# Performance work log

Hardware: AMD Instinct MI355X
Metric: run time of the kernel (lower is better)

The kernel has to match this reference:

```python
import jax, jax.numpy as jnp
import numpy as np

B, S, H, L = 1, 2048, 2048, 2
NH, D_NOPE, D_ROPE, D_V = 16, 128, 64, 128
Q_RANK, KV_RANK = 1024, 512
E, K_TOP, I_FF, N_SHARED = 8, 2, 1408, 2
VOCAB, P_DIM = 32000, 4096
EPS = 1e-6
ROPE_BASE = 10000.0
D_QK = D_NOPE + D_ROPE  # 192


def rmsnorm(x, w):
    xf = x.astype(jnp.float32)
    var = jnp.mean(xf * xf, axis=-1, keepdims=True)
    return (w * (xf * jax.lax.rsqrt(var + EPS))).astype(x.dtype)


def rotate_half(x):
    d = x.shape[-1] // 2
    return jnp.concatenate([-x[..., d:], x[..., :d]], axis=-1)


def rope_tables(seq_len):
    inv_freq = 1.0 / (ROPE_BASE ** (jnp.arange(0, D_ROPE, 2, dtype=jnp.float32) / D_ROPE))
    t = jnp.arange(seq_len, dtype=jnp.float32)
    freqs = jnp.outer(t, inv_freq)                      # [S, D_ROPE/2]
    emb = jnp.concatenate([freqs, freqs], axis=-1)      # [S, D_ROPE]
    return jnp.cos(emb)[None, None], jnp.sin(emb)[None, None]  # [1,1,S,D_ROPE]


def mla_attention(x, qd, qn, qu, kvd, kvn, kvu, ow, cos, sin):
    b, s, _ = x.shape
    # low-rank Q path
    q = rmsnorm(x @ qd, qn) @ qu                        # [B,S,NH*D_QK]
    q = q.reshape(b, s, NH, D_QK).transpose(0, 2, 1, 3)  # [B,NH,S,D_QK]
    q_nope, q_rope = q[..., :D_NOPE], q[..., D_NOPE:]
    # low-rank KV path
    kv = x @ kvd                                        # [B,S,KV_RANK+D_ROPE]
    kv_latent, k_rope = kv[..., :KV_RANK], kv[..., KV_RANK:]
    kv_up = rmsnorm(kv_latent, kvn) @ kvu               # [B,S,NH*(D_NOPE+D_V)]
    kv_up = kv_up.reshape(b, s, NH, D_NOPE + D_V)
    k_nope = kv_up[..., :D_NOPE].transpose(0, 2, 1, 3)  # [B,NH,S,D_NOPE]
    v = kv_up[..., D_NOPE:].transpose(0, 2, 1, 3)       # [B,NH,S,D_V]
    k_rope = k_rope[:, None]                            # [B,1,S,D_ROPE] broadcast over heads
    q_rope = q_rope * cos + rotate_half(q_rope) * sin
    k_rope = k_rope * cos + rotate_half(k_rope) * sin
    k_rope = jnp.broadcast_to(k_rope, (b, NH, s, D_ROPE))
    q_f = jnp.concatenate([q_nope, q_rope], axis=-1)
    k_f = jnp.concatenate([k_nope, k_rope], axis=-1)
    scores = jnp.einsum('bhqd,bhkd->bhqk', q_f, k_f) / jnp.sqrt(jnp.float32(D_QK))
    attn = jax.nn.softmax(scores.astype(jnp.float32), axis=-1).astype(x.dtype)
    out = jnp.einsum('bhqk,bhkd->bhqd', attn, v)        # [B,NH,S,D_V]
    out = out.transpose(0, 2, 1, 3).reshape(b, s, NH * D_V)
    return out @ ow


def moe_ffn(x, gw, rw1, rw2, rw3, sw1, sw2, sw3):
    b, s, h = x.shape
    xf = x.reshape(-1, h)                               # [T,H]
    T = xf.shape[0]
    # shared experts (always-on, SwiGLU)
    g_sh = jax.nn.silu(jnp.einsum('th,ehi->tei', xf, sw1)) * jnp.einsum('th,ehi->tei', xf, sw3)
    shared = jnp.einsum('tei,eih->th', g_sh, sw2)
    # routing: softmax -> top-k -> renormalize -> dense combine weights
    probs = jax.nn.softmax(xf @ gw, axis=-1)            # [T,E]
    vals, idx = jax.lax.top_k(probs, K_TOP)             # [T,K]
    vals = vals / jnp.sum(vals, axis=-1, keepdims=True)
    combine = jnp.zeros((T, E), xf.dtype).at[jnp.arange(T)[:, None], idx].add(vals)
    # routed experts (dense dispatch reference)
    g = jax.nn.silu(jnp.einsum('th,ehi->tei', xf, rw1)) * jnp.einsum('th,ehi->tei', xf, rw3)
    g = g * combine[:, :, None]
    routed = jnp.einsum('tei,eih->th', g, rw2)
    return (shared + routed).reshape(b, s, h)


def model_forward(embed, ln1_w, q_down_w, q_norm_w, q_up_w, kv_down_w, kv_norm_w,
                  kv_up_w, o_proj_w, ln2_w, gate_w, r_w1, r_w2, r_w3,
                  s_w1, s_w2, s_w3, final_norm_w, latent_q, pq_w, pk_w, pv_w,
                  po_w, pool_norm_w, input_ids):
    h = embed[input_ids]                                # [B,S,H]
    cos, sin = rope_tables(h.shape[1])
    for l in range(L):
        h = h + mla_attention(rmsnorm(h, ln1_w[l]), q_down_w[l], q_norm_w[l],
                              q_up_w[l], kv_down_w[l], kv_norm_w[l], kv_up_w[l],
                              o_proj_w[l], cos, sin)
        h = h + moe_ffn(rmsnorm(h, ln2_w[l]), gate_w[l], r_w1[l], r_w2[l], r_w3[l],
                        s_w1[l], s_w2[l], s_w3[l])
    h = rmsnorm(h, final_norm_w)
    # latent attention pooling (NV-Embed style cross attention)
    b = h.shape[0]
    q = jnp.broadcast_to(latent_q, (b, 1, H)) @ pq_w    # [B,1,H]
    k = h @ pk_w                                        # [B,S,H]
    v = h @ pv_w
    scores = jnp.einsum('bqh,bsh->bqs', q, k) / jnp.sqrt(jnp.float32(H))
    w = jax.nn.softmax(scores, axis=-1)
    pooled = jnp.einsum('bqs,bsh->bqh', w, v)[:, 0]     # [B,H]
    pooled = rmsnorm(pooled, pool_norm_w)
    return pooled @ po_w                                # [B,P_DIM]


def setup_inputs() -> dict:
    key = jax.random.key(0)
    ks = jax.random.split(key, 24)
    s = 0.02
    d = {
        'embed':      jax.random.normal(ks[0], (VOCAB, H)) * s,
        'ln1_w':      jnp.ones((L, H)),
        'q_down_w':   jax.random.normal(ks[1], (L, H, Q_RANK)) * s,
        'q_norm_w':   jnp.ones((L, Q_RANK)),
        'q_up_w':     jax.random.normal(ks[2], (L, Q_RANK, NH * D_QK)) * s,
        'kv_down_w':  jax.random.normal(ks[3], (L, H, KV_RANK + D_ROPE)) * s,
        'kv_norm_w':  jnp.ones((L, KV_RANK)),
        'kv_up_w':    jax.random.normal(ks[4], (L, KV_RANK, NH * (D_NOPE + D_V))) * s,
        'o_proj_w':   jax.random.normal(ks[5], (L, NH * D_V, H)) * s,
        'ln2_w':      jnp.ones((L, H)),
        'gate_w':     jax.random.normal(ks[6], (L, H, E)) * s,
        'r_w1':       jax.random.normal(ks[7], (L, E, H, I_FF)) * s,
        'r_w2':       jax.random.normal(ks[8], (L, E, I_FF, H)) * s,
        'r_w3':       jax.random.normal(ks[9], (L, E, H, I_FF)) * s,
        's_w1':       jax.random.normal(ks[10], (L, N_SHARED, H, I_FF)) * s,
        's_w2':       jax.random.normal(ks[11], (L, N_SHARED, I_FF, H)) * s,
        's_w3':       jax.random.normal(ks[12], (L, N_SHARED, H, I_FF)) * s,
        'final_norm_w': jnp.ones((H,)),
        'latent_q':   jax.random.normal(ks[13], (1, 1, H)),
        'pq_w':       jax.random.normal(ks[14], (H, H)) * s,
        'pk_w':       jax.random.normal(ks[15], (H, H)) * s,
        'pv_w':       jax.random.normal(ks[16], (H, H)) * s,
        'po_w':       jax.random.normal(ks[17], (H, P_DIM)) * s,
        'pool_norm_w': jnp.ones((H,)),
        'input_ids':  jax.random.randint(ks[18], (B, S), 0, VOCAB),
    }
    return d


def reference(embed, ln1_w, q_down_w, q_norm_w, q_up_w, kv_down_w, kv_norm_w,
              kv_up_w, o_proj_w, ln2_w, gate_w, r_w1, r_w2, r_w3,
              s_w1, s_w2, s_w3, final_norm_w, latent_q, pq_w, pk_w, pv_w,
              po_w, pool_norm_w, input_ids):
    return model_forward(embed, ln1_w, q_down_w, q_norm_w, q_up_w, kv_down_w,
                         kv_norm_w, kv_up_w, o_proj_w, ln2_w, gate_w, r_w1, r_w2,
                         r_w3, s_w1, s_w2, s_w3, final_norm_w, latent_q, pq_w,
                         pk_w, pv_w, po_w, pool_norm_w, input_ids)
```

## Files before the change

kernel.cpp:

```cpp
#include <hip/hip_runtime.h>
#include <hip/hip_bf16.h>

#define S_LEN  2048
#define HDIM   2048
#define NH_    16
#define DQK_   192
#define QRANK_ 1024
#define KVRANK_ 512
#define KVDN   576
#define DCAT   1600
#define KVUPN  4096
#define QN_    3072
#define IFF_   1408
#define IFF2   2816
#define EXP_   8
#define PD_    4096

typedef __attribute__((ext_vector_type(8))) short   short8_t;
typedef __attribute__((ext_vector_type(8))) __bf16  bf16x8_t;
typedef __attribute__((ext_vector_type(4))) float   f32x4;

static __device__ __forceinline__ float b2f(short s) {
  unsigned int u = ((unsigned int)(unsigned short)s) << 16;
  return __builtin_bit_cast(float, u);
// ... 30 lines not shown
  if (tid == 0) *flag = (red[0] > 1600) ? 1 : 0;
}

__global__ void __launch_bounds__(256)
convert_kernel(const void* src, short* dst, long long nchunks, const int* flag) {
  long long idx = (long long)blockIdx.x * 256 + threadIdx.x;
  long long stride = (long long)gridDim.x * 256;
  if (*flag) {
    const f32x4* s = (const f32x4*)src;
    for (long long c = idx; c < nchunks; c += stride) {
      f32x4 a = s[2 * c], b = s[2 * c + 1];
      short8_t o;
      #pragma unroll
      for (int j = 0; j < 4; ++j) { o[j] = f2b(a[j]); o[4 + j] = f2b(b[j]); }
      reinterpret_cast<short8_t*>(dst)[c] = o;
    }
  } else {
    const short8_t* s = (const short8_t*)src;
    for (long long c = idx; c < nchunks; c += stride)
      reinterpret_cast<short8_t*>(dst)[c] = s[c];
  }
}

__global__ void __launch_bounds__(256)
transconv_kernel(const void* src, short* dst, int R, int C, const int* flag,
                 long long sSrc, long long sDst, int rowMul, int rowOff) {
  long long zs = (long long)blockIdx.z * sSrc;
  long long zd = (long long)blockIdx.z * sDst;
  int r0 = blockIdx.y * 32, c0 = blockIdx.x * 32;
  int tx = threadIdx.x & 31, ty = threadIdx.x >> 5;
  __shared__ short tile[32][33];
  if (*flag) {
    const float* s = (const float*)src + zs;
    #pragma unroll
    for (int i = 0; i < 4; ++i)
      tile[ty + i * 8][tx] = f2b(s[(long long)(r0 + ty + i * 8) * C + c0 + tx]);
  } else {
    const short* s = (const short*)src + zs;
    #pragma unroll
    for (int i = 0; i < 4; ++i)
      tile[ty + i * 8][tx] = s[(long long)(r0 + ty + i * 8) * C + c0 + tx];
  }
  __syncthreads();
  short* d = dst + zd;
  #pragma unroll
  for (int i = 0; i < 4; ++i)
    d[(long long)((c0 + ty + i * 8) * rowMul + rowOff) * R + r0 + tx] = tile[tx][ty + i * 8];
}

__global__ void __launch_bounds__(256)
embed_convert_kernel(const int* ids, const void* emb, const int* flag, short* h) {
  int s = blockIdx.x;
  long long row = ids[s];
  int c = threadIdx.x;
  short8_t o;
  if (*flag) {
    const f32x4* src = (const f32x4*)((const float*)emb + row * HDIM);
    f32x4 a = src[2 * c], b = src[2 * c + 1];
    #pragma unroll
    for (int j = 0; j < 4; ++j) { o[j] = f2b(a[j]); o[4 + j] = f2b(b[j]); }
  } else {
    o = reinterpret_cast<const short8_t*>((const short*)emb + row * HDIM)[c];
  }
  reinterpret_cast<short8_t*>(h + (long long)s * HDIM)[c] = o;
}

template<int EPI>
__global__ void __launch_bounds__(256)
gemm_kernel(const short* __restrict__ A, const short* __restrict__ B,
            short* __restrict__ Cv, int M, int N, int K,
            int lda, int ldb, int ldc,
            long long sAb, long long sBb, long long sCb)
{
  __shared__ short smem[24576];
  short* shA = smem;
  short* shB = smem + 12288;
  const int tid = threadIdx.x;
  const long long bz = blockIdx.z;
  const short* Ab = A + bz * sAb;
  const short* Bb = B + bz * sBb;
  const int m0 = blockIdx.x * 128;
  const int n0 = blockIdx.y * 128;
  const int w = tid >> 6, lane = tid & 63;
  const int wm = (w >> 1) << 6, wn = (w & 1) << 6;
  const int lr = lane & 15, g = lane >> 4;
  const int srow = lane >> 2;
  const int sunit = ((lane & 3) ^ ((lane >> 3) & 3)) << 3;
  const int rsw = ((g ^ ((lr >> 1) & 3)) << 3);
  const f32x4 vzero = {0.f, 0.f, 0.f, 0.f};
  f32x4 acc[4][4];
  #pragma unroll
  for (int i = 0; i < 4; ++i)
    #pragma unroll
    for (int j = 0; j < 4; ++j) acc[i][j] = vzero;

  const int nt = K >> 5;
#define STAGE_G(bi, kk) do { \
    _Pragma("unroll") \
    for (int r = 0; r < 2; ++r) { \
      int rowb = (w << 4) + (r << 6); \
      gload16(Ab + (long long)(m0 + rowb + srow) * lda + (kk) + sunit, &shA[(bi) * 4096 + rowb * 32]); \
      gload16(Bb + (long long)(n0 + rowb + srow) * ldb + (kk) + sunit, &shB[(bi) * 4096 + rowb * 32]); \
    } } while (0)

  STAGE_G(0, 0);
  if (nt > 1) STAGE_G(1, 32);
  int cur = 0, i2 = 2;
  for (int t = 0; t < nt; ++t) {
    if (t + 1 < nt) wait_vm4(); else wait_vm0();
    __builtin_amdgcn_s_barrier();
    if (t + 2 < nt) STAGE_G(i2, (t + 2) << 5);
    short8_t af[4];
    #pragma unroll
    for (int mi = 0; mi < 4; ++mi)
      af[mi] = *reinterpret_cast<const short8_t*>(&shA[cur * 4096 + (wm + (mi << 4) + lr) * 32 + rsw]);
    __builtin_amdgcn_s_setprio(1);
    #pragma unroll
    for (int ni = 0; ni < 4; ++ni) {
      short8_t bfr = *reinterpret_cast<const short8_t*>(&shB[cur * 4096 + (wn + (ni << 4) + lr) * 32 + rsw]);
      #pragma unroll
      for (int mi = 0; mi < 4; ++mi)
        acc[mi][ni] = __builtin_amdgcn_mfma_f32_16x16x32_bf16(
            __builtin_bit_cast(bf16x8_t, af[mi]),
            __builtin_bit_cast(bf16x8_t, bfr),
            acc[mi][ni], 0, 0, 0);
    }
    __builtin_amdgcn_s_setprio(0);
    cur = (cur == 2) ? 0 : cur + 1;
    i2  = (i2 == 2) ? 0 : i2 + 1;
  }
#undef STAGE_G
  __syncthreads();
  #pragma unroll
  for (int ni = 0; ni < 4; ++ni)
    #pragma unroll
    for (int mi = 0; mi < 4; ++mi)
      #pragma unroll
      for (int r = 0; r < 4; ++r)
        smem[(wm + (mi << 4) + (g << 2) + r) * 136 + wn + (ni << 4) + lr] = f2b(acc[mi][ni][r]);
  __syncthreads();
  {
    short* C = Cv + bz * sCb;
    int row = tid >> 1, half = (tid & 1) << 6;
    if (EPI == 1) {
      int ocol = (n0 >> 1) + (half >> 1);
      #pragma unroll
      for (int j = 0; j < 4; ++j) {
        short8_t v0 = *reinterpret_cast<const short8_t*>(&smem[row * 136 + half + (j << 4)]);
        short8_t v1 = *reinterpret_cast<const short8_t*>(&smem[row * 136 + half + (j << 4) + 8]);
        short8_t o;
        #pragma unroll
        for (int q = 0; q < 4; ++q) {
          float x = b2f(v0[2 * q]);
          o[q] = f2b((x / (1.0f + expf(-x))) * b2f(v0[2 * q + 1]));
          float y = b2f(v1[2 * q]);
          o[4 + q] = f2b((y / (1.0f + expf(-y))) * b2f(v1[2 * q + 1]));
        }
        *reinterpret_cast<short8_t*>(&C[(long long)(m0 + row) * ldc + ocol + (j << 3)]) = o;
      }
    } else {
      #pragma unroll
      for (int j = 0; j < 8; ++j) {
        int col = n0 + half + (j << 3);
        if (col + 8 <= N) {
          short8_t v = *reinterpret_cast<const short8_t*>(&smem[row * 136 + half + (j << 3)]);
          short* cp = &C[(long long)(m0 + row) * ldc + col];
          if (EPI == 2) {
            short8_t hv = *reinterpret_cast<const short8_t*>(cp);
            short8_t o;
            #pragma unroll
            for (int q = 0; q < 8; ++q) o[q] = f2b(b2f(hv[q]) + b2f(v[q]));
            *reinterpret_cast<short8_t*>(cp) = o;
          } else {
            *reinterpret_cast<short8_t*>(cp) = v;
          }
        }
      }
    }
  }
}

template<int GATHER, int SILU>
__global__ void __launch_bounds__(256)
moe_gemm_kernel(const short* __restrict__ A, const int* __restrict__ elist,
                const int* __restrict__ cnt, const short* __restrict__ B,
                short* __restrict__ C, const float* __restrict__ ewt,
                int N, int K, int lda, int ldb, int ldc,
                long long sAe, long long sBe, long long sCe)
{
  const int e = blockIdx.z;
  const int cnt_e = cnt[e];
  const int m0 = blockIdx.y << 7;
  if (m0 >= cnt_e) return;
  const short* Bb = B + (long long)e * sBe;
  short* Cb = C + (long long)e * sCe;
  const int n0 = blockIdx.x << 7;
  const int tid = threadIdx.x;
  const int w = tid >> 6, lane = tid & 63;
  const int wm = (w >> 1) << 6, wn = (w & 1) << 6;
  const int lr = lane & 15, g = lane >> 4;
  const int srow = lane >> 2;
  const int sunit = ((lane & 3) ^ ((lane >> 3) & 3)) << 3;
  const int rsw = ((g ^ ((lr >> 1) & 3)) << 3);

  long long arow[2];
  #pragma unroll
  for (int r = 0; r < 2; ++r) {
    int row = m0 + (w << 4) + (r << 6) + srow;
    if (GATHER) {
      int p = row > cnt_e - 1 ? cnt_e - 1 : row;
      arow[r] = (long long)elist[e * S_LEN + p] * lda;
    } else {
      arow[r] = (long long)e * sAe + (long long)row * lda;
    }
  }

  __shared__ short smem[24576];
  short* shA = smem;
  short* shB = smem + 12288;
  const f32x4 vzero = {0.f, 0.f, 0.f, 0.f};
  f32x4 acc[4][4];
  #pragma unroll
  for (int i = 0; i < 4; ++i)
    #pragma unroll
    for (int j = 0; j < 4; ++j) acc[i][j] = vzero;

  const int nt = K >> 5;
#define STAGE_M(bi, kk) do { \
    _Pragma("unroll") \
    for (int r = 0; r < 2; ++r) { \
      int rowb = (w << 4) + (r << 6); \
      gload16(A + arow[r] + (kk) + sunit, &shA[(bi) * 4096 + rowb * 32]); \
      gload16(Bb + (long long)(n0 + rowb + srow) * ldb + (kk) + sunit, &shB[(bi) * 4096 + rowb * 32]); \
    } } while (0)

  STAGE_M(0, 0);
  if (nt > 1) STAGE_M(1, 32);
  int cur = 0, i2 = 2;
  for (int t = 0; t < nt; ++t) {
    if (t + 1 < nt) wait_vm4(); else wait_vm0();
    __builtin_amdgcn_s_barrier();
    if (t + 2 < nt) STAGE_M(i2, (t + 2) << 5);
    short8_t af[4];
    #pragma unroll
    for (int mi = 0; mi < 4; ++mi)
      af[mi] = *reinterpret_cast<const short8_t*>(&shA[cur * 4096 + (wm + (mi << 4) + lr) * 32 + rsw]);
    __builtin_amdgcn_s_setprio(1);
    #pragma unroll
    for (int ni = 0; ni < 4; ++ni) {
      short8_t bfr = *reinterpret_cast<const short8_t*>(&shB[cur * 4096 + (wn + (ni << 4) + lr) * 32 + rsw]);
      #pragma unroll
      for (int mi = 0; mi < 4; ++mi)
        acc[mi][ni] = __builtin_amdgcn_mfma_f32_16x16x32_bf16(
            __builtin_bit_cast(bf16x8_t, af[mi]),
            __builtin_bit_cast(bf16x8_t, bfr),
            acc[mi][ni], 0, 0, 0);
    }
    __builtin_amdgcn_s_setprio(0);
    cur = (cur == 2) ? 0 : cur + 1;
    i2  = (i2 == 2) ? 0 : i2 + 1;
  }
#undef STAGE_M
  __syncthreads();
  #pragma unroll
  for (int ni = 0; ni < 4; ++ni)
    #pragma unroll
    for (int mi = 0; mi < 4; ++mi)
      #pragma unroll
      for (int r = 0; r < 4; ++r)
        smem[(wm + (mi << 4) + (g << 2) + r) * 136 + wn + (ni << 4) + lr] = f2b(acc[mi][ni][r]);
  __syncthreads();
  {
    int row = tid >> 1, half = (tid & 1) << 6;
    if (m0 + row < cnt_e) {
      if (SILU) {
        float scale = ewt[e * S_LEN + m0 + row];
        int ocol = (n0 >> 1) + (half >> 1);
        #pragma unroll
        for (int j = 0; j < 4; ++j) {
          short8_t v0 = *reinterpret_cast<const short8_t*>(&smem[row * 136 + half + (j << 4)]);
          short8_t v1 = *reinterpret_cast<const short8_t*>(&smem[row * 136 + half + (j << 4) + 8]);
          short8_t o;
          #pragma unroll
          for (int q = 0; q < 4; ++q) {
            float x = b2f(v0[2 * q]);
            o[q] = f2b((x / (1.0f + expf(-x))) * b2f(v0[2 * q + 1]) * scale);
            float y = b2f(v1[2 * q]);
            o[4 + q] = f2b((y / (1.0f + expf(-y))) * b2f(v1[2 * q + 1]) * scale);
          }
          *reinterpret_cast<short8_t*>(&Cb[(long long)(m0 + row) * ldc + ocol + (j << 3)]) = o;
        }
      } else {
        #pragma unroll
        for (int j = 0; j < 8; ++j) {
          int col = n0 + half + (j << 3);
          short8_t v = *reinterpret_cast<const short8_t*>(&smem[row * 136 + half + (j << 3)]);
          *reinterpret_cast<short8_t*>(&Cb[(long long)(m0 + row) * ldc + col]) = v;
        }
      }
    }
  }
}

__global__ void __launch_bounds__(256, 1)
flash_kernel(const short* __restrict__ qf, const short* __restrict__ kf,
             const short* __restrict__ vT, short* __restrict__ ao, float scale)
{
  __shared__ short smem[59392];
  const int tid = threadIdx.x;
  const int h = blockIdx.y;
  const int q0 = blockIdx.x << 7;
  const int w = tid >> 6, lane = tid & 63;
  const int lr = lane & 15, g = lane >> 4;
  const int rb = w << 5;
  const int srow = lane >> 2;
  const int sunit = ((lane & 3) ^ ((lane >> 3) & 3)) << 3;
  const int rsw = ((g ^ ((lr >> 1) & 3)) << 3);
  const short* qh = qf + (long long)h * S_LEN * DQK_;
  const short* kh = kf + (long long)h * S_LEN * DQK_;
  const short* vh = vT + (long long)h * 128 * S_LEN;

  #pragma unroll
  for (int i = 0; i < 12; ++i) {
    int c = tid + (i << 8);
    int row = c / 24, cc = c % 24;
    int dchunk = (cc & ~3) | ((cc & 3) ^ ((row >> 1) & 3));
    *reinterpret_cast<short8_t*>(&smem[row * 200 + (dchunk << 3)]) =
        *reinterpret_cast<const short8_t*>(qh + (long long)(q0 + row) * DQK_ + (cc << 3));
  }

  const f32x4 vzero = {0.f, 0.f, 0.f, 0.f};
  f32x4 oacc[2][8];
  #pragma unroll
  for (int mi = 0; mi < 2; ++mi)
    #pragma unroll
    for (int ni = 0; ni < 8; ++ni) oacc[mi][ni] = vzero;
  float mrow[2][4], lrow[2][4];
  #pragma unroll
  for (int mi = 0; mi < 2; ++mi)
    #pragma unroll
    for (int rr = 0; rr < 4; ++rr) { mrow[mi][rr] = -3e38f; lrow[mi][rr] = 0.f; }

  __syncthreads();

  for (int kt = 0; kt < 16; ++kt) {
    const short* kbase = kh + (long long)(kt << 7) * DQK_;
    f32x4 sacc[2][8];
    #pragma unroll
    for (int mi = 0; mi < 2; ++mi)
      #pragma unroll
      for (int ni = 0; ni < 8; ++ni) sacc[mi][ni] = vzero;
#define STAGE_K(bi, kk) do { \
    _Pragma("unroll") \
    for (int r = 0; r < 2; ++r) { \
      int rowb = (w << 4) + (r << 6); \
      gload16(kbase + (long long)(rowb + srow) * DQK_ + (kk) * 32 + sunit, \
              &smem[25600 + (bi) * 4096 + rowb * 32]); \
    } } while (0)
    STAGE_K(0, 0);
    for (int ks = 0; ks < 6; ++ks) {
      if (ks < 5) { STAGE_K((ks + 1) & 1, ks + 1); wait_vm2(); }
      else wait_vm0();
      __builtin_amdgcn_s_barrier();
      const int kb = 25600 + (ks & 1) * 4096;
      short8_t aq[2];
      #pragma unroll
      for (int mi = 0; mi < 2; ++mi)
        aq[mi] = *reinterpret_cast<const short8_t*>(
            &smem[(rb + (mi << 4) + lr) * 200 + ks * 32 + rsw]);
      __builtin_amdgcn_s_setprio(1);
      #pragma unroll
      for (int ni = 0; ni < 8; ++ni) {
        short8_t bk = *reinterpret_cast<const short8_t*>(&smem[kb + ((ni << 4) + lr) * 32 + rsw]);
        #pragma unroll
        for (int mi = 0; mi < 2; ++mi)
          sacc[mi][ni] = __builtin_amdgcn_mfma_f32_16x16x32_bf16(
              __builtin_bit_cast(bf16x8_t, aq[mi]),
              __builtin_bit_cast(bf16x8_t, bk),
              sacc[mi][ni], 0, 0, 0);
      }
      __builtin_amdgcn_s_setprio(0);
      __builtin_amdgcn_s_barrier();
    }
#undef STAGE_K
    #pragma unroll
    for (int mi = 0; mi < 2; ++mi) {
      #pragma unroll
      for (int rr = 0; rr < 4; ++rr) {
        float sv[8];
        float mx = -3e38f;
        #pragma unroll
        for (int ni = 0; ni < 8; ++ni) {
          sv[ni] = b2f(f2b(sacc[mi][ni][rr])) * scale;
          mx = fmaxf(mx, sv[ni]);
        }
        #pragma unroll
        for (int d = 1; d < 16; d <<= 1) mx = fmaxf(mx, __shfl_xor(mx, d, 64));
        float mnew = fmaxf(mrow[mi][rr], mx);
        float corr = expf(mrow[mi][rr] - mnew);
        float psum = 0.f;
        short pb[8];
        #pragma unroll
        for (int ni = 0; ni < 8; ++ni) {
          float p = expf(sv[ni] - mnew);
          pb[ni] = f2b(p);
          psum += p;
        }
        #pragma unroll
        for (int d = 1; d < 16; d <<= 1) psum += __shfl_xor(psum, d, 64);
        lrow[mi][rr] = lrow[mi][rr] * corr + psum;
        mrow[mi][rr] = mnew;
        int row = rb + (mi << 4) + (g << 2) + rr;
        int xr = (row >> 1) & 3;
        #pragma unroll
        for (int ni = 0; ni < 8; ++ni) {
          int cc = (ni << 4) + lr;
          int scc = (cc & ~31) | (((((cc >> 3) & 3) ^ xr)) << 3) | (cc & 7);
          smem[33792 + row * 136 + scc] = pb[ni];
        }
        #pragma unroll
        for (int ni = 0; ni < 8; ++ni) oacc[mi][ni][rr] *= corr;
      }
    }
    __syncthreads();
    const short* vbase = vh + (kt << 7);
#define STAGE_V(bi, kk) do { \
    _Pragma("unroll") \
    for (int r = 0; r < 2; ++r) { \
      int rowb = (w << 4) + (r << 6); \
      gload16(vbase + (long long)(rowb + srow) * S_LEN + (kk) * 32 + sunit, \
              &smem[51200 + (bi) * 4096 + rowb * 32]); \
    } } while (0)
    STAGE_V(0, 0);
    for (int ks = 0; ks < 4; ++ks) {
      if (ks < 3) { STAGE_V((ks + 1) & 1, ks + 1); wait_vm2(); }
      else wait_vm0();
      __builtin_amdgcn_s_barrier();
      const int vb = 51200 + (ks & 1) * 4096;
      short8_t ap[2];
      #pragma unroll
      for (int mi = 0; mi < 2; ++mi)
        ap[mi] = *reinterpret_cast<const short8_t*>(
            &smem[33792 + (rb + (mi << 4) + lr) * 136 + ks * 32 + rsw]);
      __builtin_amdgcn_s_setprio(1);
      #pragma unroll
      for (int ni = 0; ni < 8; ++ni) {
        short8_t bv = *reinterpret_cast<const short8_t*>(&smem[vb + ((ni << 4) + lr) * 32 + rsw]);
        #pragma unroll
        for (int mi = 0; mi < 2; ++mi)
          oacc[mi][ni] = __builtin_amdgcn_mfma_f32_16x16x32_bf16(
              __builtin_bit_cast(bf16x8_t, ap[mi]),
              __builtin_bit_cast(bf16x8_t, bv),
              oacc[mi][ni], 0, 0, 0);
      }
      __builtin_amdgcn_s_setprio(0);
      __builtin_amdgcn_s_barrier();
    }
#undef STAGE_V
  }
  __syncthreads();
  #pragma unroll
  for (int mi = 0; mi < 2; ++mi)
    #pragma unroll
    for (int ni = 0; ni < 8; ++ni)
      #pragma unroll
      for (int rr = 0; rr < 4; ++rr) {
        int row = rb + (mi << 4) + (g << 2) + rr;
        smem[33792 + row * 136 + (ni << 4) + lr] = f2b(oacc[mi][ni][rr] / lrow[mi][rr]);
      }
  __syncthreads();
  {
    int row = tid >> 1, half = (tid & 1) << 6;
    #pragma unroll
    for (int j = 0; j < 8; ++j) {
      short8_t v = *reinterpret_cast<const short8_t*>(&smem[33792 + row * 136 + half + (j << 3)]);
      *reinterpret_cast<short8_t*>(&ao[(long long)(q0 + row) * HDIM + (h << 7) + half + (j << 3)]) = v;
    }
  }
}

__global__ void __launch_bounds__(64)
rope_tables_kernel(float* cosT, float* sinT) {
  int s = blockIdx.x, j = threadIdx.x;
  int i = j & 31;
  float inv = powf(10000.0f, -((float)(2 * i) / 64.0f));
  float ang = (float)s * inv;
  cosT[s * 64 + j] = cosf(ang);
  sinT[s * 64 + j] = sinf(ang);
}

__global__ void __launch_bounds__(256)
rmsnorm_bf16_kernel(const short* __restrict__ in, long long istride,
                    const short* __restrict__ w,
                    short* __restrict__ out, long long ostride, int D) {
  const short* x = in + (long long)blockIdx.x * istride;
  short* o = out + (long long)blockIdx.x * ostride;
  const int nc = D >> 3;
  float ss = 0.f;
  for (int c = threadIdx.x; c < nc; c += 256) {
    short8_t v = reinterpret_cast<const short8_t*>(x)[c];
    #pragma unroll
    for (int j = 0; j < 8; ++j) { float f = b2f(v[j]); ss += f * f; }
  }
  __shared__ float red[256];
  red[threadIdx.x] = ss; __syncthreads();
  for (int s2 = 128; s2 > 0; s2 >>= 1) {
    if (threadIdx.x < s2) red[threadIdx.x] += red[threadIdx.x + s2];
    __syncthreads();
  }
  float r = 1.0f / sqrtf(red[0] / (float)D + 1e-6f);
  for (int c = threadIdx.x; c < nc; c += 256) {
    short8_t v = reinterpret_cast<const short8_t*>(x)[c];
    short8_t wv = reinterpret_cast<const short8_t*>(w)[c];
    short8_t ov;
    #pragma unroll
    for (int j = 0; j < 8; ++j) ov[j] = f2b(b2f(wv[j]) * (b2f(v[j]) * r));
    reinterpret_cast<short8_t*>(o)[c] = ov;
  }
}

__global__ void __launch_bounds__(256)
build_qf_kernel(const short* q, const float* cosT, const float* sinT, short* qf) {
  int s = blockIdx.x;
  for (int idx = threadIdx.x; idx < NH_ * DQK_; idx += 256) {
    int h = idx / DQK_, d = idx - h * DQK_;
    const short* qr = q + (long long)s * QN_ + h * DQK_;
    float val;
    if (d < 128) val = b2f(qr[d]);
    else {
      int j = d - 128;
      float c = cosT[s * 64 + j], sn = sinT[s * 64 + j];
      float x0 = b2f(qr[128 + j]);
      float rot = (j < 32) ? -b2f(qr[128 + j + 32]) : b2f(qr[128 + j - 32]);
      val = x0 * c + rot * sn;
    }
    qf[(long long)h * S_LEN * DQK_ + (long long)s * DQK_ + d] = f2b(val);
  }
}

__global__ void __launch_bounds__(256)
build_kf_kernel(const short* kvup, const short* krope, long long kstride,
                const float* cosT, const float* sinT, short* kf) {
  int s = blockIdx.x;
  for (int idx = threadIdx.x; idx < NH_ * DQK_; idx += 256) {
    int h = idx / DQK_, d = idx - h * DQK_;
    float val;
    if (d < 128) val = b2f(kvup[(long long)s * KVUPN + h * 256 + d]);
    else {
      int j = d - 128;
      float c = cosT[s * 64 + j], sn = sinT[s * 64 + j];
      const short* kr = krope + (long long)s * kstride;
      float x0 = b2f(kr[j]);
      float rot = (j < 32) ? -b2f(kr[j + 32]) : b2f(kr[j - 32]);
      val = x0 * c + rot * sn;
    }
    kf[(long long)h * S_LEN * DQK_ + (long long)s * DQK_ + d] = f2b(val);
  }
}

__global__ void __launch_bounds__(256)
transpose_v_kernel(const short* kvup, short* vT) {
  int h = blockIdx.z;
  int r0 = blockIdx.y * 32, c0 = blockIdx.x * 32;
  int tx = threadIdx.x & 31, ty = threadIdx.x >> 5;
  __shared__ short tile[32][33];
  #pragma unroll
  for (int i = 0; i < 4; ++i)
    tile[ty + i * 8][tx] =
        kvup[(long long)(r0 + ty + i * 8) * KVUPN + h * 256 + 128 + c0 + tx];
  __syncthreads();
  short* d = vT + (long long)h * 128 * S_LEN;
  #pragma unroll
  for (int i = 0; i < 4; ++i)
    d[(long long)(c0 + ty + i * 8) * S_LEN + r0 + tx] = tile[tx][ty + i * 8];
}

__global__ void __launch_bounds__(256)
gate_kernel(const short* x2, const short* gw, int* cnt, int* elist, float* ewt, int* tok2slot) {
  int t = blockIdx.x;
  int e = threadIdx.x >> 5, j = threadIdx.x & 31;
  const short* x = x2 + (long long)t * HDIM;
  float acc = 0.f;
  for (int k = j; k < HDIM; k += 32) acc += b2f(x[k]) * b2f(gw[(long long)k * EXP_ + e]);
  __shared__ float red[8][32];
  red[e][j] = acc; __syncthreads();
  for (int s2 = 16; s2 > 0; s2 >>= 1) {
    if (j < s2) red[e][j] += red[e][j + s2];
    __syncthreads();
  }
  if (threadIdx.x == 0) {
    float l[8], p[8];
    float m = -1e30f;
    for (int q = 0; q < 8; ++q) { l[q] = b2f(f2b(red[q][0])); m = fmaxf(m, l[q]); }
    float sum = 0.f;
    for (int q = 0; q < 8; ++q) { p[q] = expf(l[q] - m); sum += p[q]; }
    int i0 = 0; for (int q = 1; q < 8; ++q) if (p[q] > p[i0]) i0 = q;
    int i1 = (i0 == 0) ? 1 : 0;
    for (int q = 0; q < 8; ++q) if (q != i0 && p[q] > p[i1]) i1 = q;
    float denom = p[i0] + p[i1];
    float w0 = b2f(f2b(p[i0] / denom));
    float w1 = b2f(f2b(p[i1] / denom));
    int pos0 = atomicAdd(&cnt[i0], 1);
    int pos1 = atomicAdd(&cnt[i1], 1);
    elist[i0 * S_LEN + pos0] = t;  ewt[i0 * S_LEN + pos0] = w0;
    elist[i1 * S_LEN + pos1] = t;  ewt[i1 * S_LEN + pos1] = w1;
    int4* slot = (int4*)tok2slot;
    slot[t] = make_int4(i0, pos0, i1, pos1);
  }
}

__global__ void __launch_bounds__(256)
moe_combine_kernel(short* h, const short* shared_out, const short* routed,
                   const int* tok2slot) {
  int t = blockIdx.x;
  const int4 sl = ((const int4*)tok2slot)[t];
  const short8_t* s0 = reinterpret_cast<const short8_t*>(shared_out + (long long)t * HDIM);
  const short8_t* s1 = reinterpret_cast<const short8_t*>(shared_out + ((long long)S_LEN + t) * HDIM);
  const short8_t* r0 = reinterpret_cast<const short8_t*>(
      routed + ((long long)sl.x * S_LEN + sl.y) * HDIM);
  const short8_t* r1 = reinterpret_cast<const short8_t*>(
      routed + ((long long)sl.z * S_LEN + sl.w) * HDIM);
  long long c = (long long)t * 256 + threadIdx.x;
  short8_t hv = reinterpret_cast<short8_t*>(h)[c];
  short8_t a0 = s0[threadIdx.x], a1 = s1[threadIdx.x];
  short8_t v0 = r0[threadIdx.x], v1 = r1[threadIdx.x];
  short8_t ov;
  #pragma unroll
  for (int j = 0; j < 8; ++j)
    ov[j] = f2b(b2f(hv[j]) + (b2f(a0[j]) + b2f(a1[j]) + b2f(v0[j]) + b2f(v1[j])));
  reinterpret_cast<short8_t*>(h)[c] = ov;
}

template<int AF32, int OUTBF16>
__global__ void __launch_bounds__(256)
gemv_bt_kernel(const void* a, const short* __restrict__ BT, void* out, int K) {
  int n = blockIdx.x;
  const short8_t* row = reinterpret_cast<const short8_t*>(BT + (long long)n * K);
  float acc = 0.f;
  for (int c = threadIdx.x; c < (K >> 3); c += 256) {
    short8_t v = row[c];
    if (AF32) {
      f32x4 a0 = reinterpret_cast<const f32x4*>(a)[2 * c];
      f32x4 a1 = reinterpret_cast<const f32x4*>(a)[2 * c + 1];
      #pragma unroll
      for (int j = 0; j < 4; ++j) {
        acc += a0[j] * b2f(v[j]);
        acc += a1[j] * b2f(v[4 + j]);
      }
    } else {
      short8_t av = reinterpret_cast<const short8_t*>(a)[c];
      #pragma unroll
      for (int j = 0; j < 8; ++j) acc += b2f(av[j]) * b2f(v[j]);
    }
  }
  __shared__ float red[256];
  red[threadIdx.x] = acc; __syncthreads();
  for (int s2 = 128; s2 > 0; s2 >>= 1) {
    if (threadIdx.x < s2) red[threadIdx.x] += red[threadIdx.x + s2];
    __syncthreads();
  }
  if (threadIdx.x == 0) {
    if (OUTBF16) ((short*)out)[n] = f2b(red[0]);
    else         ((float*)out)[n] = red[0];
  }
}

__global__ void __launch_bounds__(256)
pool_score_kernel(const short* qv, const short* kmat, float* score) {
  int s = blockIdx.x;
  const short8_t* kr = reinterpret_cast<const short8_t*>(kmat + (long long)s * HDIM);
  const short8_t* qr = reinterpret_cast<const short8_t*>(qv);
  short8_t kv8 = kr[threadIdx.x], qv8 = qr[threadIdx.x];
  float acc = 0.f;
  #pragma unroll
  for (int j = 0; j < 8; ++j) acc += b2f(qv8[j]) * b2f(kv8[j]);
  __shared__ float red[256];
  red[threadIdx.x] = acc; __syncthreads();
  for (int s2 = 128; s2 > 0; s2 >>= 1) {
    if (threadIdx.x < s2) red[threadIdx.x] += red[threadIdx.x + s2];
    __syncthreads();
  }
  if (threadIdx.x == 0) score[s] = b2f(f2b(red[0])) * 0.022097086912079608f;
}

__global__ void __launch_bounds__(256)
softmax_vec_kernel(float* v) {
  int tid = threadIdx.x;
  float f[8]; float m = -1e30f;
  #pragma unroll
  for (int i = 0; i < 8; ++i) { f[i] = v[i * 256 + tid]; m = fmaxf(m, f[i]); }
  __shared__ float red[256];
  red[tid] = m; __syncthreads();
  for (int s2 = 128; s2 > 0; s2 >>= 1) {
    if (tid < s2) red[tid] = fmaxf(red[tid], red[tid + s2]);
    __syncthreads();
  }
  m = red[0]; __syncthreads();
  float sum = 0.f;
  #pragma unroll
  for (int i = 0; i < 8; ++i) { f[i] = expf(f[i] - m); sum += f[i]; }
  red[tid] = sum; __syncthreads();
  for (int s2 = 128; s2 > 0; s2 >>= 1) {
    if (tid < s2) red[tid] += red[tid + s2];
    __syncthreads();
  }
  float inv = 1.0f / red[0];
  #pragma unroll
  for (int i = 0; i < 8; ++i) v[i * 256 + tid] = f[i] * inv;
}

__global__ void __launch_bounds__(256)
pool_wsum_t_kernel(const float* w, const short* vT, float* pooled) {
  int h = blockIdx.x;
  const short8_t* row = reinterpret_cast<const short8_t*>(vT + (long long)h * S_LEN);
  int c = threadIdx.x;
  short8_t v = row[c];
  f32x4 w0 = reinterpret_cast<const f32x4*>(w)[2 * c];
  f32x4 w1 = reinterpret_cast<const f32x4*>(w)[2 * c + 1];
  float acc = 0.f;
  #pragma unroll
  for (int j = 0; j < 4; ++j) {
    acc += w0[j] * b2f(v[j]);
    acc += w1[j] * b2f(v[4 + j]);
  }
  __shared__ float red[256];
  red[threadIdx.x] = acc; __syncthreads();
  for (int s2 = 128; s2 > 0; s2 >>= 1) {
    if (threadIdx.x < s2) red[threadIdx.x] += red[threadIdx.x + s2];
    __syncthreads();
  }
  if (threadIdx.x == 0) pooled[h] = red[0];
}

__global__ void __launch_bounds__(256)
rmsnorm_f32_kernel(const float* x, const short* w, float* out) {
  int tid = threadIdx.x;
  float f[8]; float ss = 0.f;
  #pragma unroll
  for (int i = 0; i < 8; ++i) { f[i] = x[i * 256 + tid]; ss += f[i] * f[i]; }
  __shared__ float red[256];
  red[tid] = ss; __syncthreads();
  for (int s2 = 128; s2 > 0; s2 >>= 1) {
    if (tid < s2) red[tid] += red[tid + s2];
    __syncthreads();
  }
  float r = 1.0f / sqrtf(red[0] / 2048.0f + 1e-6f);
  #pragma unroll
  for (int i = 0; i < 8; ++i) out[i * 256 + tid] = b2f(w[i * 256 + tid]) * (f[i] * r);
}

extern "C" void kernel_launch(void* const* d_in, const int* in_sizes, int n_in,
                              void* d_out, int out_size, void* d_ws, size_t ws_size,
                              hipStream_t stream)
{
  (void)n_in; (void)out_size; (void)ws_size;
  const int* ids = (const int*)d_in[24];

  char* base = (char*)d_ws;
  size_t off = 0;
  auto alloc = [&](size_t bytes) -> void* {
    void* p = base + off;
    off += (bytes + 255) & ~(size_t)255;
    return p;
  };

  int* dflag = (int*)alloc(256);

  short* qkvdwT = (short*)alloc((size_t)2 * DCAT * HDIM * 2);
  short* quwT  = (short*)alloc((size_t)2 * QN_ * QRANK_ * 2);
  short* kvuwT = (short*)alloc((size_t)2 * KVUPN * KVRANK_ * 2);
  short* opwT  = (short*)alloc((size_t)2 * HDIM * HDIM * 2);
  short* rw13T = (short*)alloc((size_t)16 * IFF2 * HDIM * 2);
  short* rw2T  = (short*)alloc((size_t)16 * HDIM * IFF_ * 2);
  short* sw13T = (short*)alloc((size_t)4 * IFF2 * HDIM * 2);
  short* sw2T  = (short*)alloc((size_t)4 * HDIM * IFF_ * 2);
  short* pqwT  = (short*)alloc((size_t)HDIM * HDIM * 2);
  short* pkwT  = (short*)alloc((size_t)HDIM * HDIM * 2);
  short* pvwT  = (short*)alloc((size_t)HDIM * HDIM * 2);
  short* powT  = (short*)alloc((size_t)PD_ * HDIM * 2);
  short* ln1w = (short*)alloc((size_t)in_sizes[1] * 2);
  short* qnw  = (short*)alloc((size_t)in_sizes[3] * 2);
  short* kvnw = (short*)alloc((size_t)in_sizes[6] * 2);
  short* ln2w = (short*)alloc((size_t)in_sizes[9] * 2);
  short* gatw = (short*)alloc((size_t)in_sizes[10] * 2);
  short* fnww = (short*)alloc((size_t)in_sizes[17] * 2);
  short* lqw  = (short*)alloc((size_t)in_sizes[18] * 2);
  short* pnww = (short*)alloc((size_t)in_sizes[23] * 2);

  float* cosT    = (float*)alloc((size_t)S_LEN * 64 * 4);
  float* sinT    = (float*)alloc((size_t)S_LEN * 64 * 4);
  short* hbuf    = (short*)alloc((size_t)S_LEN * HDIM * 2);
  short* xbuf    = (short*)alloc((size_t)S_LEN * HDIM * 2);
  short* dcat    = (short*)alloc((size_t)S_LEN * DCAT * 2);
  short* qlatn   = (short*)alloc((size_t)S_LEN * QRANK_ * 2);
  short* qbuf    = (short*)alloc((size_t)S_LEN * QN_ * 2);
  short* kvn     = (short*)alloc((size_t)S_LEN * KVRANK_ * 2);
  short* kvup    = (short*)alloc((size_t)S_LEN * KVUPN * 2);
  short* qf      = (short*)alloc((size_t)NH_ * S_LEN * DQK_ * 2);
  short* kf      = (short*)alloc((size_t)NH_ * S_LEN * DQK_ * 2);
  short* vT      = (short*)alloc((size_t)NH_ * 128 * S_LEN * 2);
  short* ao      = (short*)alloc((size_t)S_LEN * HDIM * 2);
  short* hfin    = (short*)alloc((size_t)S_LEN * HDIM * 2);
  short* kpool   = (short*)alloc((size_t)S_LEN * HDIM * 2);
  short* vpoolT  = (short*)alloc((size_t)HDIM * S_LEN * 2);
  short* qvec    = (short*)alloc((size_t)HDIM * 2);
  float* pscore  = (float*)alloc((size_t)S_LEN * 4);
  float* pooled  = (float*)alloc((size_t)HDIM * 4);
  float* pooledn = (float*)alloc((size_t)HDIM * 4);
  int*   ecnt    = (int*)alloc(64);
  int*   elist   = (int*)alloc((size_t)EXP_ * S_LEN * 4);
  float* ewt     = (float*)alloc((size_t)EXP_ * S_LEN * 4);
  int*   tok2slot= (int*)alloc((size_t)S_LEN * 16);
  short* gba_e   = (short*)alloc((size_t)EXP_ * S_LEN * IFF_ * 2);
  short* routed  = (short*)alloc((size_t)EXP_ * S_LEN * HDIM * 2);
  short* gsh1    = (short*)alloc((size_t)2 * S_LEN * IFF_ * 2);
  short* shared_out = (short*)alloc((size_t)2 * S_LEN * HDIM * 2);

  detect_kernel<<<1, 256, 0, stream>>>(d_in[0], dflag);

  auto tconv = [&](const void* src, short* dst, int R, int C, int nslabs,
                   long long sSrc, long long sDst, int rowMul, int rowOff) {
    dim3 grid(C / 32, R / 32, nslabs);
    transconv_kernel<<<grid, 256, 0, stream>>>(src, dst, R, C, dflag, sSrc, sDst, rowMul, rowOff);
  };
  auto pconv = [&](const void* src, short* dst, long long n) {
    long long nchunks = n / 8;
    int blocks = (int)((nchunks + 255) / 256);
    if (blocks > 2048) blocks = 2048;
    if (blocks < 1) blocks = 1;
    convert_kernel<<<blocks, 256, 0, stream>>>(src, dst, nchunks, dflag);
  };

  tconv(d_in[2], qkvdwT, HDIM, QRANK_, 2,
        (long long)HDIM * QRANK_, (long long)DCAT * HDIM, 1, 0);
  tconv(d_in[5], qkvdwT + (size_t)QRANK_ * HDIM, HDIM, KVDN, 2,
        (long long)HDIM * KVDN, (long long)DCAT * HDIM, 1, 0);
  tconv(d_in[4],  quwT,  QRANK_, QN_,  2, (long long)QRANK_ * QN_,  (long long)QN_ * QRANK_, 1, 0);
  tconv(d_in[7],  kvuwT, KVRANK_,KVUPN,2, (long long)KVRANK_ * KVUPN,(long long)KVUPN * KVRANK_, 1, 0);
  tconv(d_in[8],  opwT,  HDIM,   HDIM, 2, (long long)HDIM * HDIM,   (long long)HDIM * HDIM, 1, 0);
  tconv(d_in[11], rw13T, HDIM,   IFF_, 16,(long long)HDIM * IFF_,   (long long)IFF2 * HDIM, 2, 0);
  tconv(d_in[13], rw13T, HDIM,   IFF_, 16,(long long)HDIM * IFF_,   (long long)IFF2 * HDIM, 2, 1);
  tconv(d_in[12], rw2T,  IFF_,   HDIM, 16,(long long)IFF_ * HDIM,   (long long)HDIM * IFF_, 1, 0);
  tconv(d_in[14], sw13T, HDIM,   IFF_, 4, (long long)HDIM * IFF_,   (long long)IFF2 * HDIM, 2, 0);
  tconv(d_in[16], sw13T, HDIM,   IFF_, 4, (long long)HDIM * IFF_,   (long long)IFF2 * HDIM, 2, 1);
  tconv(d_in[15], sw2T,  IFF_,   HDIM, 4, (long long)IFF_ * HDIM,   (long long)HDIM * IFF_, 1, 0);
  tconv(d_in[19], pqwT,  HDIM,   HDIM, 1, 0, 0, 1, 0);
  tconv(d_in[20], pkwT,  HDIM,   HDIM, 1, 0, 0, 1, 0);
  tconv(d_in[21], pvwT,  HDIM,   HDIM, 1, 0, 0, 1, 0);
  tconv(d_in[22], powT,  HDIM,   PD_,  1, 0, 0, 1, 0);
  pconv(d_in[1],  ln1w, in_sizes[1]);
  pconv(d_in[3],  qnw,  in_sizes[3]);
  pconv(d_in[6],  kvnw, in_sizes[6]);
  pconv(d_in[9],  ln2w, in_sizes[9]);
  pconv(d_in[10], gatw, in_sizes[10]);
  pconv(d_in[17], fnww, in_sizes[17]);
  pconv(d_in[18], lqw,  in_sizes[18]);
  pconv(d_in[23], pnww, in_sizes[23]);

  const float qk_scale = 1.0f / sqrtf((float)DQK_);

  auto gemm = [&](int epi, const short* A, const short* B, short* C,
                  int M, int N, int K, int lda, int ldb, int ldc,
                  int batch, long long sA, long long sB, long long sC) {
    dim3 grid(M / 128, (N + 127) / 128, batch);
    if (epi == 0)
      gemm_kernel<0><<<grid, 256, 0, stream>>>(A, B, C, M, N, K, lda, ldb, ldc, sA, sB, sC);
    else if (epi == 1)
      gemm_kernel<1><<<grid, 256, 0, stream>>>(A, B, C, M, N, K, lda, ldb, ldc, sA, sB, sC);
    else
      gemm_kernel<2><<<grid, 256, 0, stream>>>(A, B, C, M, N, K, lda, ldb, ldc, sA, sB, sC);
  };

  rope_tables_kernel<<<S_LEN, 64, 0, stream>>>(cosT, sinT);
  embed_convert_kernel<<<S_LEN, 256, 0, stream>>>(ids, d_in[0], dflag, hbuf);

  for (int l = 0; l < 2; ++l) {
    const short* w_ln1  = ln1w + (size_t)l * HDIM;
    const short* w_qkvT = qkvdwT + (size_t)l * DCAT * HDIM;
    const short* w_qn   = qnw  + (size_t)l * QRANK_;
    const short* w_quT  = quwT + (size_t)l * QN_ * QRANK_;
    const short* w_kvn  = kvnw + (size_t)l * KVRANK_;
    const short* w_kvuT = kvuwT+ (size_t)l * KVUPN * KVRANK_;
    const short* w_opT  = opwT + (size_t)l * HDIM * HDIM;
    const short* w_ln2  = ln2w + (size_t)l * HDIM;
    const short* w_gat  = gatw + (size_t)l * HDIM * EXP_;

    rmsnorm_bf16_kernel<<<S_LEN, 256, 0, stream>>>(hbuf, HDIM, w_ln1, xbuf, HDIM, HDIM);
    gemm(0, xbuf, w_qkvT, dcat, S_LEN, DCAT, HDIM, HDIM, HDIM, DCAT, 1, 0, 0, 0);
    rmsnorm_bf16_kernel<<<S_LEN, 256, 0, stream>>>(dcat, DCAT, w_qn, qlatn, QRANK_, QRANK_);
    gemm(0, qlatn, w_quT, qbuf, S_LEN, QN_, QRANK_, QRANK_, QRANK_, QN_, 1, 0, 0, 0);
    rmsnorm_bf16_kernel<<<S_LEN, 256, 0, stream>>>(dcat + QRANK_, DCAT, w_kvn, kvn, KVRANK_, KVRANK_);
    gemm(0, kvn, w_kvuT, kvup, S_LEN, KVUPN, KVRANK_, KVRANK_, KVRANK_, KVUPN, 1, 0, 0, 0);
    build_qf_kernel<<<S_LEN, 256, 0, stream>>>(qbuf, cosT, sinT, qf);
    build_kf_kernel<<<S_LEN, 256, 0, stream>>>(kvup, dcat + QRANK_ + KVRANK_, DCAT, cosT, sinT, kf);
    {
      dim3 tg(128 / 32, S_LEN / 32, NH_);
      transpose_v_kernel<<<tg, 256, 0, stream>>>(kvup, vT);
    }
    {
      dim3 fg(S_LEN / 128, NH_);
      flash_kernel<<<fg, 256, 0, stream>>>(qf, kf, vT, ao, qk_scale);
    }
    gemm(2, ao, w_opT, hbuf, S_LEN, HDIM, HDIM, HDIM, HDIM, HDIM, 1, 0, 0, 0);

    rmsnorm_bf16_kernel<<<S_LEN, 256, 0, stream>>>(hbuf, HDIM, w_ln2, xbuf, HDIM, HDIM);
    hipMemsetAsync(ecnt, 0, 64, stream);
    gate_kernel<<<S_LEN, 256, 0, stream>>>(xbuf, w_gat, ecnt, elist, ewt, tok2slot);
    {
      const short* a13 = sw13T + (size_t)l * 2 * IFF2 * HDIM;
      const short* a2  = sw2T  + (size_t)l * 2 * HDIM * IFF_;
      gemm(1, xbuf, a13, gsh1, S_LEN, IFF2, HDIM, HDIM, HDIM, IFF_, 2,
           0, (long long)IFF2 * HDIM, (long long)S_LEN * IFF_);
      gemm(0, gsh1, a2, shared_out, S_LEN, HDIM, IFF_, IFF_, IFF_, HDIM, 2,
           (long long)S_LEN * IFF_, (long long)HDIM * IFF_, (long long)S_LEN * HDIM);
    }
    {
      const short* b13 = rw13T + (size_t)l * 8 * IFF2 * HDIM;
      const short* b2  = rw2T  + (size_t)l * 8 * HDIM * IFF_;
      dim3 g13(IFF2 / 128, S_LEN / 128, EXP_);
      moe_gemm_kernel<1, 1><<<g13, 256, 0, stream>>>(
          xbuf, elist, ecnt, b13, gba_e, ewt, IFF2, HDIM, HDIM, HDIM, IFF_,
          0, (long long)IFF2 * HDIM, (long long)S_LEN * IFF_);
      dim3 g2(HDIM / 128, S_LEN / 128, EXP_);
      moe_gemm_kernel<0, 0><<<g2, 256, 0, stream>>>(
          gba_e, elist, ecnt, b2, routed, nullptr, HDIM, IFF_, IFF_, IFF_, HDIM,
          (long long)S_LEN * IFF_, (long long)HDIM * IFF_, (long long)S_LEN * HDIM);
      moe_combine_kernel<<<S_LEN, 256, 0, stream>>>(hbuf, shared_out, routed, tok2slot);
    }
  }

  rmsnorm_bf16_kernel<<<S_LEN, 256, 0, stream>>>(hbuf, HDIM, fnww, hfin, HDIM, HDIM);
  gemm(0, hfin, pkwT, kpool, S_LEN, HDIM, HDIM, HDIM, HDIM, HDIM, 1, 0, 0, 0);
  gemm(0, pvwT, hfin, vpoolT, HDIM, S_LEN, HDIM, HDIM, HDIM, S_LEN, 1, 0, 0, 0);
  gemv_bt_kernel<0,1><<<HDIM, 256, 0, stream>>>(lqw, pqwT, qvec, HDIM);
  pool_score_kernel<<<S_LEN, 256, 0, stream>>>(qvec, kpool, pscore);
  softmax_vec_kernel<<<1, 256, 0, stream>>>(pscore);
  pool_wsum_t_kernel<<<HDIM, 256, 0, stream>>>(pscore, vpoolT, pooled);
  rmsnorm_f32_kernel<<<1, 256, 0, stream>>>(pooled, pnww, pooledn);
  gemv_bt_kernel<1,0><<<PD_, 256, 0, stream>>>(pooledn, powT, (float*)d_out, HDIM);
}
```

Before: 1.710 ms.

## Halve flash-attention query tile and merge shared-expert gate/up GEMMs

The flash attention kernel now processes 64 query rows per block instead of 128, with one 16-row MFMA tile per wave. This doubles the grid, cuts shared memory, and drops the single-block occupancy bound so more blocks can be resident. Each K/V tile is now staged once per 64 query rows, so global/LDS traffic per unit of work doubles. The two shared-expert gate/up GEMMs become one wider GEMM writing a concatenated buffer, and the down GEMM uses strided slices of it, which removes a batched launch dimension.

```diff
diff --git a/kernel.cpp b/kernel.cpp
--- a/kernel.cpp
+++ b/kernel.cpp
@@ -356,17 +356,17 @@
   }
 }
 
-__global__ void __launch_bounds__(256, 1)
+__global__ void __launch_bounds__(256)
 flash_kernel(const short* __restrict__ qf, const short* __restrict__ kf,
              const short* __restrict__ vT, short* __restrict__ ao, float scale)
 {
-  __shared__ short smem[59392];
+  __shared__ short smem[37888];
   const int tid = threadIdx.x;
   const int h = blockIdx.y;
-  const int q0 = blockIdx.x << 7;
+  const int q0 = blockIdx.x << 6;
   const int w = tid >> 6, lane = tid & 63;
   const int lr = lane & 15, g = lane >> 4;
-  const int rb = w << 5;
+  const int rb = w << 4;
   const int srow = lane >> 2;
   const int sunit = ((lane & 3) ^ ((lane >> 3) & 3)) << 3;
   const int rsw = ((g ^ ((lr >> 1) & 3)) << 3);
@@ -375,7 +375,7 @@
   const short* vh = vT + (long long)h * 128 * S_LEN;
 
   #pragma unroll
-  for (int i = 0; i < 12; ++i) {
+  for (int i = 0; i < 6; ++i) {
     int c = tid + (i << 8);
     int row = c / 24, cc = c % 24;
     int dchunk = (cc & ~3) | ((cc & 3) ^ ((row >> 1) & 3));
@@ -384,97 +384,83 @@
   }
 
   const f32x4 vzero = {0.f, 0.f, 0.f, 0.f};
-  f32x4 oacc[2][8];
-  #pragma unroll
-  for (int mi = 0; mi < 2; ++mi)
-    #pragma unroll
-    for (int ni = 0; ni < 8; ++ni) oacc[mi][ni] = vzero;
-  float mrow[2][4], lrow[2][4];
-  #pragma unroll
-  for (int mi = 0; mi < 2; ++mi)
-    #pragma unroll
-    for (int rr = 0; rr < 4; ++rr) { mrow[mi][rr] = -3e38f; lrow[mi][rr] = 0.f; }
+  f32x4 oacc[8];
+  #pragma unroll
+  for (int ni = 0; ni < 8; ++ni) oacc[ni] = vzero;
+  float mrow[4], lrow[4];
+  #pragma unroll
+  for (int rr = 0; rr < 4; ++rr) { mrow[rr] = -3e38f; lrow[rr] = 0.f; }
 
   __syncthreads();
 
   for (int kt = 0; kt < 16; ++kt) {
     const short* kbase = kh + (long long)(kt << 7) * DQK_;
-    f32x4 sacc[2][8];
-    #pragma unroll
-    for (int mi = 0; mi < 2; ++mi)
-      #pragma unroll
-      for (int ni = 0; ni < 8; ++ni) sacc[mi][ni] = vzero;
+    f32x4 sacc[8];
+    #pragma unroll
+    for (int ni = 0; ni < 8; ++ni) sacc[ni] = vzero;
 #define STAGE_K(bi, kk) do { \
     _Pragma("unroll") \
     for (int r = 0; r < 2; ++r) { \
       int rowb = (w << 4) + (r << 6); \
       gload16(kbase + (long long)(rowb + srow) * DQK_ + (kk) * 32 + sunit, \
-              &smem[25600 + (bi) * 4096 + rowb * 32]); \
+              &smem[12800 + (bi) * 4096 + rowb * 32]); \
     } } while (0)
     STAGE_K(0, 0);
     for (int ks = 0; ks < 6; ++ks) {
       if (ks < 5) { STAGE_K((ks + 1) & 1, ks + 1); wait_vm2(); }
       else wait_vm0();
       __builtin_amdgcn_s_barrier();
-      const int kb = 25600 + (ks & 1) * 4096;
-      short8_t aq[2];
-      #pragma unroll
-      for (int mi = 0; mi < 2; ++mi)
-        aq[mi] = *reinterpret_cast<const short8_t*>(
-            &smem[(rb + (mi << 4) + lr) * 200 + ks * 32 + rsw]);
+      const int kb = 12800 + (ks & 1) * 4096;
+      short8_t aq = *reinterpret_cast<const short8_t*>(
+          &smem[(rb + lr) * 200 + ks * 32 + rsw]);
       __builtin_amdgcn_s_setprio(1);
       #pragma unroll
       for (int ni = 0; ni < 8; ++ni) {
         short8_t bk = *reinterpret_cast<const short8_t*>(&smem[kb + ((ni << 4) + lr) * 32 + rsw]);
-        #pragma unroll
-        for (int mi = 0; mi < 2; ++mi)
-          sacc[mi][ni] = __builtin_amdgcn_mfma_f32_16x16x32_bf16(
-              __builtin_bit_cast(bf16x8_t, aq[mi]),
-              __builtin_bit_cast(bf16x8_t, bk),
-              sacc[mi][ni], 0, 0, 0);
+        sacc[ni] = __builtin_amdgcn_mfma_f32_16x16x32_bf16(
+            __builtin_bit_cast(bf16x8_t, aq),
+            __builtin_bit_cast(bf16x8_t, bk),
+            sacc[ni], 0, 0, 0);
       }
       __builtin_amdgcn_s_setprio(0);
       __builtin_amdgcn_s_barrier();
     }
 #undef STAGE_K
     #pragma unroll
-    for (int mi = 0; mi < 2; ++mi) {
-      #pragma unroll
-      for (int rr = 0; rr < 4; ++rr) {
-        float sv[8];
-        float mx = -3e38f;
-        #pragma unroll
-        for (int ni = 0; ni < 8; ++ni) {
-          sv[ni] = b2f(f2b(sacc[mi][ni][rr])) * scale;
-          mx = fmaxf(mx, sv[ni]);
-        }
-        #pragma unroll
-        for (int d = 1; d < 16; d <<= 1) mx = fmaxf(mx, __shfl_xor(mx, d, 64));
-        float mnew = fmaxf(mrow[mi][rr], mx);
-        float corr = expf(mrow[mi][rr] - mnew);
-        float psum = 0.f;
-        short pb[8];
-        #pragma unroll
-        for (int ni = 0; ni < 8; ++ni) {
-          float p = expf(sv[ni] - mnew);
-          pb[ni] = f2b(p);
-          psum += p;
-        }
-        #pragma unroll
-        for (int d = 1; d < 16; d <<= 1) psum += __shfl_xor(psum, d, 64);
-        lrow[mi][rr] = lrow[mi][rr] * corr + psum;
-        mrow[mi][rr] = mnew;
-        int row = rb + (mi << 4) + (g << 2) + rr;
-        int xr = (row >> 1) & 3;
-        #pragma unroll
-        for (int ni = 0; ni < 8; ++ni) {
-          int cc = (ni << 4) + lr;
-          int scc = (cc & ~31) | (((((cc >> 3) & 3) ^ xr)) << 3) | (cc & 7);
-          smem[33792 + row * 136 + scc] = pb[ni];
-        }
-        #pragma unroll
-        for (int ni = 0; ni < 8; ++ni) oacc[mi][ni][rr] *= corr;
+    for (int rr = 0; rr < 4; ++rr) {
+      float sv[8];
+      float mx = -3e38f;
+      #pragma unroll
+      for (int ni = 0; ni < 8; ++ni) {
+        sv[ni] = b2f(f2b(sacc[ni][rr])) * scale;
+        mx = fmaxf(mx, sv[ni]);
       }
+      #pragma unroll
+      for (int d = 1; d < 16; d <<= 1) mx = fmaxf(mx, __shfl_xor(mx, d, 64));
+      float mnew = fmaxf(mrow[rr], mx);
+      float corr = expf(mrow[rr] - mnew);
+      float psum = 0.f;
+      short pb[8];
+      #pragma unroll
+      for (int ni = 0; ni < 8; ++ni) {
+        float p = expf(sv[ni] - mnew);
+        pb[ni] = f2b(p);
+        psum += p;
+      }
+      #pragma unroll
+      for (int d = 1; d < 16; d <<= 1) psum += __shfl_xor(psum, d, 64);
+      lrow[rr] = lrow[rr] * corr + psum;
+      mrow[rr] = mnew;
+      int row = rb + (g << 2) + rr;
+      int xr = (row >> 1) & 3;
+      #pragma unroll
+      for (int ni = 0; ni < 8; ++ni) {
+        int cc = (ni << 4) + lr;
+        int scc = (cc & ~31) | (((((cc >> 3) & 3) ^ xr)) << 3) | (cc & 7);
+        smem[20992 + row * 136 + scc] = pb[ni];
+      }
+      #pragma unroll
+      for (int ni = 0; ni < 8; ++ni) oacc[ni][rr] *= corr;
     }
     __syncthreads();
     const short* vbase = vh + (kt << 7);
@@ -483,29 +469,24 @@
     for (int r = 0; r < 2; ++r) { \
       int rowb = (w << 4) + (r << 6); \
       gload16(vbase + (long long)(rowb + srow) * S_LEN + (kk) * 32 + sunit, \
-              &smem[51200 + (bi) * 4096 + rowb * 32]); \
+              &smem[29696 + (bi) * 4096 + rowb * 32]); \
     } } while (0)
     STAGE_V(0, 0);
     for (int ks = 0; ks < 4; ++ks) {
       if (ks < 3) { STAGE_V((ks + 1) & 1, ks + 1); wait_vm2(); }
       else wait_vm0();
       __builtin_amdgcn_s_barrier();
-      const int vb = 51200 + (ks & 1) * 4096;
-      short8_t ap[2];
-      #pragma unroll
-      for (int mi = 0; mi < 2; ++mi)
-        ap[mi] = *reinterpret_cast<const short8_t*>(
-            &smem[33792 + (rb + (mi << 4) + lr) * 136 + ks * 32 + rsw]);
+      const int vb = 29696 + (ks & 1) * 4096;
+      short8_t ap = *reinterpret_cast<const short8_t*>(
+          &smem[20992 + (rb + lr) * 136 + ks * 32 + rsw]);
       __builtin_amdgcn_s_setprio(1);
       #pragma unroll
       for (int ni = 0; ni < 8; ++ni) {
         short8_t bv = *reinterpret_cast<const short8_t*>(&smem[vb + ((ni << 4) + lr) * 32 + rsw]);
-        #pragma unroll
-        for (int mi = 0; mi < 2; ++mi)
-          oacc[mi][ni] = __builtin_amdgcn_mfma_f32_16x16x32_bf16(
-              __builtin_bit_cast(bf16x8_t, ap[mi]),
-              __builtin_bit_cast(bf16x8_t, bv),
-              oacc[mi][ni], 0, 0, 0);
+        oacc[ni] = __builtin_amdgcn_mfma_f32_16x16x32_bf16(
+            __builtin_bit_cast(bf16x8_t, ap),
+            __builtin_bit_cast(bf16x8_t, bv),
+            oacc[ni], 0, 0, 0);
       }
       __builtin_amdgcn_s_setprio(0);
       __builtin_amdgcn_s_barrier();
@@ -514,21 +495,20 @@
   }
   __syncthreads();
   #pragma unroll
-  for (int mi = 0; mi < 2; ++mi)
-    #pragma unroll
-    for (int ni = 0; ni < 8; ++ni)
-      #pragma unroll
-      for (int rr = 0; rr < 4; ++rr) {
-        int row = rb + (mi << 4) + (g << 2) + rr;
-        smem[33792 + row * 136 + (ni << 4) + lr] = f2b(oacc[mi][ni][rr] / lrow[mi][rr]);
-      }
+  for (int ni = 0; ni < 8; ++ni)
+    #pragma unroll
+    for (int rr = 0; rr < 4; ++rr) {
+      int row = rb + (g << 2) + rr;
+      smem[20992 + row * 136 + (ni << 4) + lr] = f2b(oacc[ni][rr] / lrow[rr]);
+    }
   __syncthreads();
   {
-    int row = tid >> 1, half = (tid & 1) << 6;
-    #pragma unroll
-    for (int j = 0; j < 8; ++j) {
-      short8_t v = *reinterpret_cast<const short8_t*>(&smem[33792 + row * 136 + half + (j << 3)]);
-      *reinterpret_cast<short8_t*>(&ao[(long long)(q0 + row) * HDIM + (h << 7) + half + (j << 3)]) = v;
+    int row = tid >> 2, quarter = (tid & 3) << 5;
+    #pragma unroll
+    for (int j = 0; j < 4; ++j) {
+      int col = quarter + (j << 3);
+      short8_t v = *reinterpret_cast<const short8_t*>(&smem[20992 + row * 136 + col]);
+      *reinterpret_cast<short8_t*>(&ao[(long long)(q0 + row) * HDIM + (h << 7) + col]) = v;
     }
   }
 }
@@ -867,7 +847,7 @@
   int*   tok2slot= (int*)alloc((size_t)S_LEN * 16);
   short* gba_e   = (short*)alloc((size_t)EXP_ * S_LEN * IFF_ * 2);
   short* routed  = (short*)alloc((size_t)EXP_ * S_LEN * HDIM * 2);
-  short* gsh1    = (short*)alloc((size_t)2 * S_LEN * IFF_ * 2);
+  short* gsh1    = (short*)alloc((size_t)S_LEN * IFF2 * 2);
   short* shared_out = (short*)alloc((size_t)2 * S_LEN * HDIM * 2);
 
   detect_kernel<<<1, 256, 0, stream>>>(d_in[0], dflag);
@@ -952,7 +932,7 @@
       transpose_v_kernel<<<tg, 256, 0, stream>>>(kvup, vT);
     }
     {
-      dim3 fg(S_LEN / 128, NH_);
+      dim3 fg(S_LEN / 64, NH_);
       flash_kernel<<<fg, 256, 0, stream>>>(qf, kf, vT, ao, qk_scale);
     }
     gemm(2, ao, w_opT, hbuf, S_LEN, HDIM, HDIM, HDIM, HDIM, HDIM, 1, 0, 0, 0);
@@ -963,10 +943,9 @@
     {
       const short* a13 = sw13T + (size_t)l * 2 * IFF2 * HDIM;
       const short* a2  = sw2T  + (size_t)l * 2 * HDIM * IFF_;
-      gemm(1, xbuf, a13, gsh1, S_LEN, IFF2, HDIM, HDIM, HDIM, IFF_, 2,
-           0, (long long)IFF2 * HDIM, (long long)S_LEN * IFF_);
-      gemm(0, gsh1, a2, shared_out, S_LEN, HDIM, IFF_, IFF_, IFF_, HDIM, 2,
-           (long long)S_LEN * IFF_, (long long)HDIM * IFF_, (long long)S_LEN * HDIM);
+      gemm(1, xbuf, a13, gsh1, S_LEN, 2 * IFF2, HDIM, HDIM, HDIM, IFF2, 1, 0, 0, 0);
+      gemm(0, gsh1, a2, shared_out, S_LEN, HDIM, IFF_, IFF2, IFF_, HDIM, 2,
+           (long long)IFF_, (long long)HDIM * IFF_, (long long)S_LEN * HDIM);
     }
     {
       const short* b13 = rw13T + (size_t)l * 8 * IFF2 * HDIM;
```

New measurement: 1.640 ms. -4.1%, faster.
